# Performance work log

Hardware: AMD Instinct MI355X
Metric: run time of the kernel (lower is better)

Reference implementation:

```python
import jax, jax.numpy as jnp
import numpy as np

COMMITMENT_COST = 0.25
NUM_EMBEDDINGS = 512
EMBEDDING_DIM = 64


def setup_inputs() -> dict:
    key = jax.random.key(0)
    k1, k2 = jax.random.split(key)
    inputs = jax.random.normal(k1, (32, EMBEDDING_DIM, 64, 64), dtype=jnp.float32)  # B,C,H,W
    embedding = jax.random.normal(k2, (NUM_EMBEDDINGS, EMBEDDING_DIM), dtype=jnp.float32)  # K,D
    return {"inputs": inputs, "embedding": embedding}


def reference(inputs, embedding):
    # Eval-mode forward of VectorQuantizerEMA (training-branch EMA updates are
    # in-place buffer updates, skipped when self.training is False).
    x = jnp.transpose(inputs, (0, 2, 3, 1))            # B,H,W,C
    B, H, W, D = x.shape
    K = embedding.shape[0]
    flat = x.reshape(-1, D)                            # N,D
    d = (jnp.sum(flat * flat, axis=1, keepdims=True)
         + jnp.sum(embedding * embedding, axis=1)
         - 2.0 * flat @ embedding.T)
    indices = jnp.argmin(d, axis=1)                    # N (int)
    # gather == one-hot @ embedding, but without materializing N x K one-hot
    quantized = embedding[indices].reshape(B, H, W, D)
    # commitment loss (quantized is detached in the torch code)
    e_latent_loss = jnp.mean((jax.lax.stop_gradient(quantized) - x) ** 2)
    loss = COMMITMENT_COST * e_latent_loss
    # straight-through estimator
    quantized_st = x + jax.lax.stop_gradient(quantized - x)
    # perplexity from encoding histogram (avg of one-hots = counts / N)
    counts = jnp.zeros((K,), dtype=flat.dtype).at[indices].add(1.0)
    avg_probs = counts / flat.shape[0]
    perplexity = jnp.exp(-jnp.sum(avg_probs * jnp.log(avg_probs + 1e-10)))
    out = jnp.transpose(quantized_st, (0, 3, 1, 2))    # B,C,H,W
    return loss, out, perplexity, indices
```

## Files before the change

kernel.cpp:

```cpp
#include <hip/hip_runtime.h>
#include <math.h>

#define NPIX   131072
#define KEMB   512
#define DDIM   64
#define HW     4096
#define BSTRIDE 262144

#define OUT_OFF  1
#define PERP_OFF 8388609
#define IDX_OFF  8388610

typedef __attribute__((ext_vector_type(8))) short bf16x8;
typedef __attribute__((ext_vector_type(4))) float f32x4;

__device__ __forceinline__ unsigned short bf16_rtne(float f) {
    unsigned int u = __float_as_uint(f);
    u += 0x7FFFu + ((u >> 16) & 1u);
    return (unsigned short)(u >> 16);
}
__device__ __forceinline__ float bf16_to_f(unsigned short h) {
    return __uint_as_float(((unsigned int)h) << 16);
}

#define MFMA_STEP(AH, AM, AL, XH, XM, XL, ACC) \
    ACC = __builtin_amdgcn_mfma_f32_16x16x32_bf16(AH, XH, ACC, 0, 0, 0); \
    ACC = __builtin_amdgcn_mfma_f32_16x16x32_bf16(AH, XM, ACC, 0, 0, 0); \
    ACC = __builtin_amdgcn_mfma_f32_16x16x32_bf16(AM, XH, ACC, 0, 0, 0); \
    ACC = __builtin_amdgcn_mfma_f32_16x16x32_bf16(AH, XL, ACC, 0, 0, 0); \
    ACC = __builtin_amdgcn_mfma_f32_16x16x32_bf16(AL, XH, ACC, 0, 0, 0); \
    ACC = __builtin_amdgcn_mfma_f32_16x16x32_bf16(AM, XM, ACC, 0, 0, 0);

__global__ void vq_init(const float* __restrict__ emb, int* __restrict__ counts,
                        float* __restrict__ hnorms, float* __restrict__ loss_acc,
                        unsigned short* __restrict__ ebh, unsigned short* __restrict__ ebm,
                        unsigned short* __restrict__ ebl) {
    const int k = blockIdx.x;
    const int c = threadIdx.x;
    float x = emb[k * DDIM + c];
    unsigned short h = bf16_rtne(x);
    float r1 = x - bf16_to_f(h);
    unsigned short m = bf16_rtne(r1);
    float r2 = r1 - bf16_to_f(m);
    unsigned short l = bf16_rtne(r2);
    ebh[k * DDIM + c] = h; ebm[k * DDIM + c] = m; ebl[k * DDIM + c] = l;
    float s = x * x;
#pragma unroll
    for (int off = 1; off <= 32; off <<= 1) s += __shfl_xor(s, off, 64);
    if (c == 0) {
        hnorms[k] = 0.5f * s;
        counts[k] = 0;
        if (k == 0) *loss_acc = 0.f;
    }
}

__global__ __launch_bounds__(1024, 4) void vq_main(
    const float* __restrict__ in, const float* __restrict__ emb,
    const unsigned short* __restrict__ ebh, const unsigned short* __restrict__ ebm,
    const unsigned short* __restrict__ ebl,
    const float* __restrict__ hnorms, int* __restrict__ counts,
    float* __restrict__ loss_acc, float* __restrict__ dout)
{
    __shared__ __align__(16) unsigned short ebh_l[KEMB * DDIM];
    __shared__ __align__(16) unsigned short ebm_l[KEMB * DDIM];
    __shared__ __align__(16) float hn_lds[KEMB];
    __shared__ int hist[KEMB];

    const int t    = threadIdx.x;
    const int lane = t & 63;
    const int wv   = t >> 6;
    const int quad = lane >> 4;
    const int col  = lane & 15;
    const int b    = blockIdx.x >> 3;
    const int p0   = ((blockIdx.x & 7) << 9) | (wv << 5);
    const float* xb = in + b * BSTRIDE;

    if (t < KEMB) hist[t] = 0;
    if (t < 128) ((float4*)hn_lds)[t] = ((const float4*)hnorms)[t];

#pragma unroll
    for (int i = 0; i < 4; ++i) {
        const int f  = t + i * 1024;
        const int ct = f >> 7;
        const int ks = (f >> 6) & 1;
        const int lf = f & 63;
        const int src = (ct * 16 + (lf & 15)) * DDIM + ks * 32 + (lf >> 4) * 8;
        const int dst = ct * 1024 + ks * 512 + lf * 8;
        *(bf16x8*)&ebh_l[dst] = *(const bf16x8*)(ebh + src);
        *(bf16x8*)&ebm_l[dst] = *(const bf16x8*)(ebm + src);
    }

    bf16x8 xf[3][2][2];
#pragma unroll
    for (int tt = 0; tt < 2; ++tt) {
#pragma unroll
        for (int s = 0; s < 2; ++s) {
            const int pp = p0 + tt * 16 + col;
            const int c0 = s * 32 + quad * 8;
            bf16x8 vh, vm, vl;
#pragma unroll
            for (int j = 0; j < 8; ++j) {
                float x = xb[(c0 + j) * HW + pp];
                unsigned short h = bf16_rtne(x);
                float r1 = x - bf16_to_f(h);
                unsigned short m = bf16_rtne(r1);
                float r2 = r1 - bf16_to_f(m);
                unsigned short l = bf16_rtne(r2);
                vh[j] = (short)h; vm[j] = (short)m; vl[j] = (short)l;
            }
            xf[0][tt][s] = vh; xf[1][tt][s] = vm; xf[2][tt][s] = vl;
        }
    }

    __syncthreads();

    const int arow = col * DDIM + quad * 8;
    float v1[2], v2[2]; int k1[2], k2[2];
#pragma unroll
    for (int tt = 0; tt < 2; ++tt) {
        v1[tt] = 3.402823466e38f; v2[tt] = 3.402823466e38f; k1[tt] = 0; k2[tt] = 0;
    }

    bf16x8 Al0 = *(const bf16x8*)(ebl + arow);
    bf16x8 Al1 = *(const bf16x8*)(ebl + arow + 32);

    for (int ct = 0; ct < 32; ++ct) {
        bf16x8 Al0n, Al1n;
        if (ct < 31) {
            const int sb = (ct + 1) * 1024 + arow;
            Al0n = *(const bf16x8*)(ebl + sb);
            Al1n = *(const bf16x8*)(ebl + sb + 32);
        }

        const int base = ct * 1024 + lane * 8;
        const bf16x8 Ah0 = *(const bf16x8*)&ebh_l[base];
        const bf16x8 Ah1 = *(const bf16x8*)&ebh_l[base + 512];
        const bf16x8 Am0 = *(const bf16x8*)&ebm_l[base];
        const bf16x8 Am1 = *(const bf16x8*)&ebm_l[base + 512];

        f32x4 acc0 = (f32x4){0.f, 0.f, 0.f, 0.f};
        f32x4 acc1 = (f32x4){0.f, 0.f, 0.f, 0.f};
        MFMA_STEP(Ah0, Am0, Al0, xf[0][0][0], xf[1][0][0], xf[2][0][0], acc0)
        MFMA_STEP(Ah1, Am1, Al1, xf[0][0][1], xf[1][0][1], xf[2][0][1], acc0)
        MFMA_STEP(Ah0, Am0, Al0, xf[0][1][0], xf[1][1][0], xf[2][1][0], acc1)
        MFMA_STEP(Ah1, Am1, Al1, xf[0][1][1], xf[1][1][1], xf[2][1][1], acc1)

        const f32x4 hn = *(const f32x4*)&hn_lds[ct * 16 + quad * 4];
#pragma unroll
        for (int r = 0; r < 4; ++r) {
            const int kk = ct * 16 + quad * 4 + r;
            float sc = hn[r] - acc0[r];
            if (sc < v1[0]) { v2[0] = v1[0]; k2[0] = k1[0]; v1[0] = sc; k1[0] = kk; }
            else if (sc < v2[0]) { v2[0] = sc; k2[0] = kk; }
            sc = hn[r] - acc1[r];
            if (sc < v1[1]) { v2[1] = v1[1]; k2[1] = k1[1]; v1[1] = sc; k1[1] = kk; }
            else if (sc < v2[1]) { v2[1] = sc; k2[1] = kk; }
        }

        Al0 = Al0n; Al1 = Al1n;
    }

#pragma unroll
    for (int tt = 0; tt < 2; ++tt) {
#pragma unroll
        for (int off = 16; off <= 32; off <<= 1) {
            float w1 = __shfl_xor(v1[tt], off, 64); int j1 = __shfl_xor(k1[tt], off, 64);
            float w2 = __shfl_xor(v2[tt], off, 64); int j2 = __shfl_xor(k2[tt], off, 64);
            bool aF = (v1[tt] < w1) || (v1[tt] == w1 && k1[tt] < j1);
            float t1 = aF ? v1[tt] : w1;  int u1 = aF ? k1[tt] : j1;
            float tl = aF ? w1 : v1[tt];  int ul = aF ? j1 : k1[tt];
            bool bS = (v2[tt] < w2) || (v2[tt] == w2 && k2[tt] < j2);
            float tc = bS ? v2[tt] : w2;  int uc = bS ? k2[tt] : j2;
            bool lS = (tl < tc) || (tl == tc && ul < uc);
            v1[tt] = t1; k1[tt] = u1;
            v2[tt] = lS ? tl : tc; k2[tt] = lS ? ul : uc;
        }
    }

    const int q    = lane & 31;
    const int pp   = p0 + q;
    const int tsel = (lane >> 4) & 1;
    const int kA = tsel ? k1[1] : k1[0];
    const int kB = tsel ? k2[1] : k2[0];

    const int kMine = (lane < 32) ? kA : kB;
    const float4* eM = (const float4*)(emb + kMine * DDIM);
    float a0 = hn_lds[kMine], a1 = 0.f, a2 = 0.f, a3 = 0.f;
#pragma unroll
    for (int i = 0; i < 16; ++i) {
        float4 ea = eM[i];
        const int c = i * 4;
        float x0 = xb[(c + 0) * HW + pp];
        float x1 = xb[(c + 1) * HW + pp];
        float x2 = xb[(c + 2) * HW + pp];
        float x3 = xb[(c + 3) * HW + pp];
        a0 = fmaf(-x0, ea.x, a0);
        a1 = fmaf(-x1, ea.y, a1);
        a2 = fmaf(-x2, ea.z, a2);
        a3 = fmaf(-x3, ea.w, a3);
    }
    const float dMine = (a0 + a1) + (a2 + a3);
    const float dOth  = __shfl_xor(dMine, 32, 64);
    const float dA = (lane < 32) ? dMine : dOth;
    const float dB = (lane < 32) ? dOth  : dMine;
    const int myk = (dB < dA || (dB == dA && kB < kA)) ? kB : kA;

    float lsum = 0.f;
    if (lane < 32) {
        dout[IDX_OFF + b * HW + pp] = (float)myk;
        atomicAdd(&hist[myk], 1);
        const float4* qrow = (const float4*)(emb + myk * DDIM);
        float* ob = dout + OUT_OFF + b * BSTRIDE;
#pragma unroll
        for (int i = 0; i < 16; ++i) {
            float4 qv = qrow[i];
            const int c = i * 4;
            float x0 = xb[(c + 0) * HW + pp];
            float x1 = xb[(c + 1) * HW + pp];
            float x2 = xb[(c + 2) * HW + pp];
            float x3 = xb[(c + 3) * HW + pp];
            float d0 = qv.x - x0;
            float d1 = qv.y - x1;
            float d2 = qv.z - x2;
            float d3 = qv.w - x3;
            lsum += d0 * d0 + d1 * d1 + d2 * d2 + d3 * d3;
            ob[(c + 0) * HW + pp] = x0 + d0;
            ob[(c + 1) * HW + pp] = x1 + d1;
            ob[(c + 2) * HW + pp] = x2 + d2;
            ob[(c + 3) * HW + pp] = x3 + d3;
        }
    }
    for (int off = 32; off > 0; off >>= 1) lsum += __shfl_down(lsum, off, 64);
    if (lane == 0) atomicAdd(loss_acc, lsum);

    __syncthreads();
    if (t < KEMB) {
        int v = hist[t];
        if (v) atomicAdd(&counts[t], v);
    }
}

__global__ void vq_fin(const int* __restrict__ counts,
                       const float* __restrict__ loss_acc,
                       float* __restrict__ dout) {
    __shared__ float part[8];
    const int k = threadIdx.x;
    float pa = (float)counts[k] / (float)NPIX;
    float v = pa * logf(pa + 1e-10f);
#pragma unroll
    for (int off = 1; off <= 32; off <<= 1) v += __shfl_xor(v, off, 64);
    if ((k & 63) == 0) part[k >> 6] = v;
    __syncthreads();
    if (k == 0) {
        float s = 0.f;
#pragma unroll
        for (int i = 0; i < 8; ++i) s += part[i];
        dout[PERP_OFF] = expf(-s);
        dout[0] = 0.25f * (*loss_acc) / 8388608.0f;
    }
}

extern "C" void kernel_launch(void* const* d_in, const int* in_sizes, int n_in,
                              void* d_out, int out_size, void* d_ws, size_t ws_size,
                              hipStream_t stream) {
    const float* in  = (const float*)d_in[0];
    const float* emb = (const float*)d_in[1];
    float* dout = (float*)d_out;
    int*   counts   = (int*)d_ws;
    float* hnorms   = (float*)((char*)d_ws + 2048);
    float* loss_acc = (float*)((char*)d_ws + 4096);
    unsigned short* ebh = (unsigned short*)((char*)d_ws + 8192);
    unsigned short* ebm = ebh + KEMB * DDIM;
    unsigned short* ebl = ebm + KEMB * DDIM;

    vq_init<<<512, 64, 0, stream>>>(emb, counts, hnorms, loss_acc, ebh, ebm, ebl);
    vq_main<<<256, 1024, 0, stream>>>(in, emb, ebh, ebm, ebl, hnorms, counts, loss_acc, dout);
    vq_fin<<<1, 512, 0, stream>>>(counts, loss_acc, dout);
}
```

Before: 175.6 us.

## Halve pixels per wave, double grid, and fuse finalize via last-block counter

```diff
diff --git a/kernel.cpp b/kernel.cpp
--- a/kernel.cpp
+++ b/kernel.cpp
@@ -33,46 +33,53 @@
 
 __global__ void vq_init(const float* __restrict__ emb, int* __restrict__ counts,
                         float* __restrict__ hnorms, float* __restrict__ loss_acc,
-                        unsigned short* __restrict__ ebh, unsigned short* __restrict__ ebm,
-                        unsigned short* __restrict__ ebl) {
+                        int* __restrict__ done_ctr,
+                        unsigned short* __restrict__ ebh_t,
+                        unsigned short* __restrict__ ebml) {
     const int k = blockIdx.x;
     const int c = threadIdx.x;
+    const int ct = k >> 4, col = k & 15;
+    const int ks = c >> 5, quad = (c >> 3) & 3, j = c & 7;
     float x = emb[k * DDIM + c];
     unsigned short h = bf16_rtne(x);
     float r1 = x - bf16_to_f(h);
     unsigned short m = bf16_rtne(r1);
     float r2 = r1 - bf16_to_f(m);
     unsigned short l = bf16_rtne(r2);
-    ebh[k * DDIM + c] = h; ebm[k * DDIM + c] = m; ebl[k * DDIM + c] = l;
+    ebh_t[ct * 1024 + ks * 512 + (quad * 16 + col) * 8 + j] = h;
+    const int mb = ct * 2048 + col * 128 + ks * 64 + quad * 8 + j;
+    ebml[mb]      = m;
+    ebml[mb + 32] = l;
     float s = x * x;
 #pragma unroll
     for (int off = 1; off <= 32; off <<= 1) s += __shfl_xor(s, off, 64);
     if (c == 0) {
         hnorms[k] = 0.5f * s;
         counts[k] = 0;
-        if (k == 0) *loss_acc = 0.f;
-    }
-}
-
-__global__ __launch_bounds__(1024, 4) void vq_main(
+        if (k == 0) { *loss_acc = 0.f; *done_ctr = 0; }
+    }
+}
+
+__global__ __launch_bounds__(1024, 8) void vq_main(
     const float* __restrict__ in, const float* __restrict__ emb,
-    const unsigned short* __restrict__ ebh, const unsigned short* __restrict__ ebm,
-    const unsigned short* __restrict__ ebl,
+    const unsigned short* __restrict__ ebh_t, const unsigned short* __restrict__ ebml,
     const float* __restrict__ hnorms, int* __restrict__ counts,
-    float* __restrict__ loss_acc, float* __restrict__ dout)
+    float* __restrict__ loss_acc, int* __restrict__ done_ctr,
+    float* __restrict__ dout)
 {
     __shared__ __align__(16) unsigned short ebh_l[KEMB * DDIM];
-    __shared__ __align__(16) unsigned short ebm_l[KEMB * DDIM];
     __shared__ __align__(16) float hn_lds[KEMB];
     __shared__ int hist[KEMB];
+    __shared__ float part[8];
+    __shared__ int lastflag;
 
     const int t    = threadIdx.x;
     const int lane = t & 63;
     const int wv   = t >> 6;
     const int quad = lane >> 4;
     const int col  = lane & 15;
-    const int b    = blockIdx.x >> 3;
-    const int p0   = ((blockIdx.x & 7) << 9) | (wv << 5);
+    const int b    = blockIdx.x >> 4;
+    const int p0   = ((blockIdx.x & 15) << 8) | (wv << 4);
     const float* xb = in + b * BSTRIDE;
 
     if (t < KEMB) hist[t] = 0;
@@ -80,108 +87,77 @@
 
 #pragma unroll
     for (int i = 0; i < 4; ++i) {
-        const int f  = t + i * 1024;
-        const int ct = f >> 7;
-        const int ks = (f >> 6) & 1;
-        const int lf = f & 63;
-        const int src = (ct * 16 + (lf & 15)) * DDIM + ks * 32 + (lf >> 4) * 8;
-        const int dst = ct * 1024 + ks * 512 + lf * 8;
-        *(bf16x8*)&ebh_l[dst] = *(const bf16x8*)(ebh + src);
-        *(bf16x8*)&ebm_l[dst] = *(const bf16x8*)(ebm + src);
-    }
-
-    bf16x8 xf[3][2][2];
-#pragma unroll
-    for (int tt = 0; tt < 2; ++tt) {
-#pragma unroll
-        for (int s = 0; s < 2; ++s) {
-            const int pp = p0 + tt * 16 + col;
-            const int c0 = s * 32 + quad * 8;
-            bf16x8 vh, vm, vl;
-#pragma unroll
-            for (int j = 0; j < 8; ++j) {
-                float x = xb[(c0 + j) * HW + pp];
-                unsigned short h = bf16_rtne(x);
-                float r1 = x - bf16_to_f(h);
-                unsigned short m = bf16_rtne(r1);
-                float r2 = r1 - bf16_to_f(m);
-                unsigned short l = bf16_rtne(r2);
-                vh[j] = (short)h; vm[j] = (short)m; vl[j] = (short)l;
-            }
-            xf[0][tt][s] = vh; xf[1][tt][s] = vm; xf[2][tt][s] = vl;
-        }
-    }
-
-    __syncthreads();
-
-    const int arow = col * DDIM + quad * 8;
-    float v1[2], v2[2]; int k1[2], k2[2];
-#pragma unroll
-    for (int tt = 0; tt < 2; ++tt) {
-        v1[tt] = 3.402823466e38f; v2[tt] = 3.402823466e38f; k1[tt] = 0; k2[tt] = 0;
-    }
-
-    bf16x8 Al0 = *(const bf16x8*)(ebl + arow);
-    bf16x8 Al1 = *(const bf16x8*)(ebl + arow + 32);
+        const int f = (t + i * 1024) * 8;
+        *(bf16x8*)&ebh_l[f] = *(const bf16x8*)(ebh_t + f);
+    }
+
+    bf16x8 xf[3][2];
+#pragma unroll
+    for (int s = 0; s < 2; ++s) {
+        const int ppb = p0 + col;
+        const int c0  = s * 32 + quad * 8;
+        bf16x8 vh, vm, vl;
+#pragma unroll
+        for (int j = 0; j < 8; ++j) {
+            float x = xb[(c0 + j) * HW + ppb];
+            unsigned short h = bf16_rtne(x);
+            float r1 = x - bf16_to_f(h);
+            unsigned short m = bf16_rtne(r1);
+            float r2 = r1 - bf16_to_f(m);
+            unsigned short l = bf16_rtne(r2);
+            vh[j] = (short)h; vm[j] = (short)m; vl[j] = (short)l;
+        }
+        xf[0][s] = vh; xf[1][s] = vm; xf[2][s] = vl;
+    }
+
+    __syncthreads();
+
+    float v1 = 3.402823466e38f, v2 = 3.402823466e38f;
+    int   k1 = 0, k2 = 0;
+    const char* ap = (const char*)ebml + col * 256 + quad * 16;
 
     for (int ct = 0; ct < 32; ++ct) {
-        bf16x8 Al0n, Al1n;
-        if (ct < 31) {
-            const int sb = (ct + 1) * 1024 + arow;
-            Al0n = *(const bf16x8*)(ebl + sb);
-            Al1n = *(const bf16x8*)(ebl + sb + 32);
-        }
+        const bf16x8 Am0 = *(const bf16x8*)(ap);
+        const bf16x8 Al0 = *(const bf16x8*)(ap + 64);
+        const bf16x8 Am1 = *(const bf16x8*)(ap + 128);
+        const bf16x8 Al1 = *(const bf16x8*)(ap + 192);
+        ap += 4096;
 
         const int base = ct * 1024 + lane * 8;
         const bf16x8 Ah0 = *(const bf16x8*)&ebh_l[base];
         const bf16x8 Ah1 = *(const bf16x8*)&ebh_l[base + 512];
-        const bf16x8 Am0 = *(const bf16x8*)&ebm_l[base];
-        const bf16x8 Am1 = *(const bf16x8*)&ebm_l[base + 512];
-
-        f32x4 acc0 = (f32x4){0.f, 0.f, 0.f, 0.f};
-        f32x4 acc1 = (f32x4){0.f, 0.f, 0.f, 0.f};
-        MFMA_STEP(Ah0, Am0, Al0, xf[0][0][0], xf[1][0][0], xf[2][0][0], acc0)
-        MFMA_STEP(Ah1, Am1, Al1, xf[0][0][1], xf[1][0][1], xf[2][0][1], acc0)
-        MFMA_STEP(Ah0, Am0, Al0, xf[0][1][0], xf[1][1][0], xf[2][1][0], acc1)
-        MFMA_STEP(Ah1, Am1, Al1, xf[0][1][1], xf[1][1][1], xf[2][1][1], acc1)
+
+        f32x4 acc = (f32x4){0.f, 0.f, 0.f, 0.f};
+        MFMA_STEP(Ah0, Am0, Al0, xf[0][0], xf[1][0], xf[2][0], acc)
+        MFMA_STEP(Ah1, Am1, Al1, xf[0][1], xf[1][1], xf[2][1], acc)
 
         const f32x4 hn = *(const f32x4*)&hn_lds[ct * 16 + quad * 4];
 #pragma unroll
         for (int r = 0; r < 4; ++r) {
             const int kk = ct * 16 + quad * 4 + r;
-            float sc = hn[r] - acc0[r];
-            if (sc < v1[0]) { v2[0] = v1[0]; k2[0] = k1[0]; v1[0] = sc; k1[0] = kk; }
-            else if (sc < v2[0]) { v2[0] = sc; k2[0] = kk; }
-            sc = hn[r] - acc1[r];
-            if (sc < v1[1]) { v2[1] = v1[1]; k2[1] = k1[1]; v1[1] = sc; k1[1] = kk; }
-            else if (sc < v2[1]) { v2[1] = sc; k2[1] = kk; }
-        }
-
-        Al0 = Al0n; Al1 = Al1n;
-    }
-
-#pragma unroll
-    for (int tt = 0; tt < 2; ++tt) {
-#pragma unroll
-        for (int off = 16; off <= 32; off <<= 1) {
-            float w1 = __shfl_xor(v1[tt], off, 64); int j1 = __shfl_xor(k1[tt], off, 64);
-            float w2 = __shfl_xor(v2[tt], off, 64); int j2 = __shfl_xor(k2[tt], off, 64);
-            bool aF = (v1[tt] < w1) || (v1[tt] == w1 && k1[tt] < j1);
-            float t1 = aF ? v1[tt] : w1;  int u1 = aF ? k1[tt] : j1;
-            float tl = aF ? w1 : v1[tt];  int ul = aF ? j1 : k1[tt];
-            bool bS = (v2[tt] < w2) || (v2[tt] == w2 && k2[tt] < j2);
-            float tc = bS ? v2[tt] : w2;  int uc = bS ? k2[tt] : j2;
-            bool lS = (tl < tc) || (tl == tc && ul < uc);
-            v1[tt] = t1; k1[tt] = u1;
-            v2[tt] = lS ? tl : tc; k2[tt] = lS ? ul : uc;
-        }
-    }
-
-    const int q    = lane & 31;
+            float sc = hn[r] - acc[r];
+            if (sc < v1) { v2 = v1; k2 = k1; v1 = sc; k1 = kk; }
+            else if (sc < v2) { v2 = sc; k2 = kk; }
+        }
+    }
+
+#pragma unroll
+    for (int off = 16; off <= 32; off <<= 1) {
+        float w1 = __shfl_xor(v1, off, 64); int j1 = __shfl_xor(k1, off, 64);
+        float w2 = __shfl_xor(v2, off, 64); int j2 = __shfl_xor(k2, off, 64);
+        bool aF = (v1 < w1) || (v1 == w1 && k1 < j1);
+        float t1 = aF ? v1 : w1;  int u1 = aF ? k1 : j1;
+        float tl = aF ? w1 : v1;  int ul = aF ? j1 : k1;
+        bool bS = (v2 < w2) || (v2 == w2 && k2 < j2);
+        float tc = bS ? v2 : w2;  int uc = bS ? k2 : j2;
+        bool lS = (tl < tc) || (tl == tc && ul < uc);
+        v1 = t1; k1 = u1;
+        v2 = lS ? tl : tc; k2 = lS ? ul : uc;
+    }
+
+    const int q    = lane & 15;
     const int pp   = p0 + q;
-    const int tsel = (lane >> 4) & 1;
-    const int kA = tsel ? k1[1] : k1[0];
-    const int kB = tsel ? k2[1] : k2[0];
+    const int kA   = k1, kB = k2;
 
     const int kMine = (lane < 32) ? kA : kB;
     const float4* eM = (const float4*)(emb + kMine * DDIM);
@@ -206,7 +182,7 @@
     const int myk = (dB < dA || (dB == dA && kB < kA)) ? kB : kA;
 
     float lsum = 0.f;
-    if (lane < 32) {
+    if (lane < 16) {
         dout[IDX_OFF + b * HW + pp] = (float)myk;
         atomicAdd(&hist[myk], 1);
         const float4* qrow = (const float4*)(emb + myk * DDIM);
@@ -238,25 +214,28 @@
         int v = hist[t];
         if (v) atomicAdd(&counts[t], v);
     }
-}
-
-__global__ void vq_fin(const int* __restrict__ counts,
-                       const float* __restrict__ loss_acc,
-                       float* __restrict__ dout) {
-    __shared__ float part[8];
-    const int k = threadIdx.x;
-    float pa = (float)counts[k] / (float)NPIX;
-    float v = pa * logf(pa + 1e-10f);
-#pragma unroll
-    for (int off = 1; off <= 32; off <<= 1) v += __shfl_xor(v, off, 64);
-    if ((k & 63) == 0) part[k >> 6] = v;
-    __syncthreads();
-    if (k == 0) {
-        float s = 0.f;
-#pragma unroll
-        for (int i = 0; i < 8; ++i) s += part[i];
-        dout[PERP_OFF] = expf(-s);
-        dout[0] = 0.25f * (*loss_acc) / 8388608.0f;
+
+    __threadfence();
+    __syncthreads();
+    if (t == 0) lastflag = (atomicAdd(done_ctr, 1) == 511) ? 1 : 0;
+    __syncthreads();
+    if (lastflag) {
+        if (t < KEMB) {
+            int cnt = atomicAdd(&counts[t], 0);
+            float pa = (float)cnt / (float)NPIX;
+            float v = pa * logf(pa + 1e-10f);
+#pragma unroll
+            for (int off = 1; off <= 32; off <<= 1) v += __shfl_xor(v, off, 64);
+            if ((t & 63) == 0) part[t >> 6] = v;
+        }
+        __syncthreads();
+        if (t == 0) {
+            float s = 0.f;
+#pragma unroll
+            for (int i = 0; i < 8; ++i) s += part[i];
+            dout[PERP_OFF] = expf(-s);
+            dout[0] = 0.25f * atomicAdd(loss_acc, 0.0f) / 8388608.0f;
+        }
     }
 }
 
@@ -269,11 +248,10 @@
     int*   counts   = (int*)d_ws;
     float* hnorms   = (float*)((char*)d_ws + 2048);
     float* loss_acc = (float*)((char*)d_ws + 4096);
-    unsigned short* ebh = (unsigned short*)((char*)d_ws + 8192);
-    unsigned short* ebm = ebh + KEMB * DDIM;
-    unsigned short* ebl = ebm + KEMB * DDIM;
-
-    vq_init<<<512, 64, 0, stream>>>(emb, counts, hnorms, loss_acc, ebh, ebm, ebl);
-    vq_main<<<256, 1024, 0, stream>>>(in, emb, ebh, ebm, ebl, hnorms, counts, loss_acc, dout);
-    vq_fin<<<1, 512, 0, stream>>>(counts, loss_acc, dout);
-}
+    int*   done_ctr = (int*)((char*)d_ws + 4160);
+    unsigned short* ebh_t = (unsigned short*)((char*)d_ws + 8192);
+    unsigned short* ebml  = ebh_t + KEMB * DDIM;
+
+    vq_init<<<512, 64, 0, stream>>>(emb, counts, hnorms, loss_acc, done_ctr, ebh_t, ebml);
+    vq_main<<<512, 1024, 0, stream>>>(in, emb, ebh_t, ebml, hnorms, counts, loss_acc, done_ctr, dout);
+}
```

After: 479.2 us. 2.73x slower.
